# Kernel optimization log

Hardware: AMD Instinct MI355X
Metric: run time of the kernel (lower is better)

Reference implementation:

```python
import jax, jax.numpy as jnp
import numpy as np


def setup_inputs() -> dict:
    key = jax.random.key(0)
    k1, k2, k3, k4 = jax.random.split(key, 4)
    B, S, D, R = 8, 1024, 1024, 256
    batch = jax.random.normal(k1, (B, S, D), dtype=jnp.float32)
    proj_L = jax.random.uniform(k2, (D, R), dtype=jnp.float32, minval=-0.05, maxval=0.05)
    proj_R = jax.random.uniform(k3, (R, D), dtype=jnp.float32, minval=-0.05, maxval=0.05)
    bias = jax.random.uniform(k4, (1,), dtype=jnp.float32, minval=-0.05, maxval=0.05)
    return {"batch": batch, "proj_L": proj_L, "proj_R": proj_R, "bias": bias}


def reference(batch, proj_L, proj_R, bias):
    # logits[b,i,j] = h_i^T (L @ R) h_j + bias
    # Efficient factored form (same math, avoids O(B*S^2*D) intermediates):
    # left[b,i,r] = (batch @ L)[b,i,r]; right[b,j,r] = (batch @ R^T)[b,j,r]
    left = jnp.einsum('bid,dr->bir', batch, proj_L)    # (B,S,R)
    right = jnp.einsum('bjd,rd->bjr', batch, proj_R)   # (B,S,R)
    logits = jnp.einsum('bir,bjr->bij', left, right) + bias[0]
    return logits
```

## Files before the change

kernel.cpp:

```cpp
#include <hip/hip_runtime.h>

typedef __bf16 bf16_t;
typedef __bf16 bf16x8 __attribute__((ext_vector_type(8)));
typedef __bf16 bf16x4 __attribute__((ext_vector_type(4)));
typedef float f32x4 __attribute__((ext_vector_type(4)));

__device__ __forceinline__ void async16(const void* g, void* l) {
  __builtin_amdgcn_global_load_lds(
      (const __attribute__((address_space(1))) unsigned int*)g,
      (__attribute__((address_space(3))) unsigned int*)l,
      16, 0, 0);
}

__device__ __forceinline__ bf16x8 cvt8(const float4 a, const float4 b) {
  bf16x8 v;
  v[0] = (bf16_t)a.x; v[1] = (bf16_t)a.y; v[2] = (bf16_t)a.z; v[3] = (bf16_t)a.w;
  v[4] = (bf16_t)b.x; v[5] = (bf16_t)b.y; v[6] = (bf16_t)b.z; v[7] = (bf16_t)b.w;
  return v;
}

__global__ void prep_Bcat(const float* __restrict__ projL,
                          const float* __restrict__ projR,
                          bf16_t* __restrict__ Bcat) {
  const int t = threadIdx.x;
  if (blockIdx.x < 256) {
    int i = blockIdx.x * 256 + t;
    float4 v = ((const float4*)projR)[i];
    bf16x4 o;
    o[0] = (bf16_t)v.x; o[1] = (bf16_t)v.y; o[2] = (bf16_t)v.z; o[3] = (bf16_t)v.w;
    ((bf16x4*)(Bcat + (long)256 * 1024))[i] = o;
  } else {
    __shared__ float tile[32][33];
    const int bb = blockIdx.x - 256;
    const int n0 = (bb & 7) * 32;
    const int k0 = (bb >> 3) * 32;
    const int tx = t & 31;
    const int ty = t >> 5;
#pragma unroll
    for (int i = 0; i < 32; i += 8)
      tile[ty + i][tx] = projL[(long)(k0 + ty + i) * 256 + n0 + tx];
    __syncthreads();
#pragma unroll
    for (int i = 0; i < 32; i += 8)
      Bcat[(long)(n0 + ty + i) * 1024 + k0 + tx] = (bf16_t)tile[tx][ty + i];
  }
}

__global__ __launch_bounds__(256, 2) void gemm1_fusedA(
    const float* __restrict__ batch, const bf16_t* __restrict__ Bcat,
    bf16_t* __restrict__ LR) {
  const int bx = blockIdx.x;
  const int tm = (bx & 127) * 64;
  const int tn = (bx >> 7) * 128;

  __shared__ __attribute__((aligned(16))) bf16_t Bs[2 * 16384];

  const int t = threadIdx.x;
  const int lane = t & 63;
  const int quad = lane >> 4;
  const int l15 = lane & 15;
  const int wave = t >> 6;
  const int wr = (wave >> 1) * 32;
  const int wc = (wave & 1) * 64;

  const int rS = t >> 2;
  const int cS = (t & 3) * 8;
  const bf16_t* gB = Bcat + (long)(tn + rS) * 1024 + cS;

  const float* gA = batch + (long)(tm + wr + l15) * 1024 + quad * 8;

  f32x4 acc[2][4];
#pragma unroll
  for (int i = 0; i < 2; ++i)
#pragma unroll
    for (int j = 0; j < 4; ++j)
      acc[i][j] = (f32x4){0.f, 0.f, 0.f, 0.f};

#pragma unroll
  for (int kc = 0; kc < 4; ++kc) {
    async16(gB + kc * 32, Bs + kc * 4096 + t * 8);
    async16(gB + kc * 32 + (long)64 * 1024, Bs + kc * 4096 + 2048 + t * 8);
  }
  __syncthreads();

  for (int s = 0; s < 8; ++s) {
    const int buf = s & 1;
    const int nb = buf ^ 1;
    const int k0 = s * 128;
    if (s < 7) {
#pragma unroll
      for (int kc = 0; kc < 4; ++kc) {
        async16(gB + k0 + 128 + kc * 32, Bs + nb * 16384 + kc * 4096 + t * 8);
        async16(gB + k0 + 128 + kc * 32 + (long)64 * 1024,
                Bs + nb * 16384 + kc * 4096 + 2048 + t * 8);
      }
    }
    float4 a0[4][2], a1[4][2];
#pragma unroll
    for (int kc = 0; kc < 4; ++kc) {
      const float* p0 = gA + k0 + kc * 32;
      a0[kc][0] = *(const float4*)p0;
      a0[kc][1] = *(const float4*)(p0 + 4);
      const float* p1 = p0 + (long)16 * 1024;
      a1[kc][0] = *(const float4*)p1;
      a1[kc][1] = *(const float4*)(p1 + 4);
    }
#pragma unroll
    for (int kc = 0; kc < 4; ++kc) {
      bf16x8 af[2], bv[4];
      af[0] = cvt8(a0[kc][0], a0[kc][1]);
      af[1] = cvt8(a1[kc][0], a1[kc][1]);
      const bf16_t* Bk = Bs + buf * 16384 + kc * 4096;
#pragma unroll
      for (int j = 0; j < 4; ++j)
        bv[j] = *(const bf16x8*)(Bk + (wc + j * 16 + l15) * 32 + quad * 8);
#pragma unroll
      for (int i = 0; i < 2; ++i)
#pragma unroll
        for (int j = 0; j < 4; ++j)
          acc[i][j] = __builtin_amdgcn_mfma_f32_16x16x32_bf16(af[i], bv[j],
                                                              acc[i][j], 0, 0, 0);
    }
    __syncthreads();
  }

#pragma unroll
  for (int i = 0; i < 2; ++i) {
    const int r0 = tm + wr + i * 16 + quad * 4;
#pragma unroll
    for (int j = 0; j < 4; ++j) {
      const int c0 = tn + wc + j * 16 + l15;
#pragma unroll
      for (int r = 0; r < 4; ++r)
        LR[(long)(r0 + r) * 512 + c0] = (bf16_t)acc[i][j][r];
    }
  }
}

__global__ __launch_bounds__(256, 2) void gemm2(const bf16_t* __restrict__ LR,
                                                float* __restrict__ out,
                                                const float* __restrict__ bias) {
  const int bx = blockIdx.x;
  const int bz = bx & 7;
  const int tile = bx >> 3;
  const int tm = (tile & 7) * 128;
  const int tn = (tile >> 3) * 128;
  const bf16_t* LRb = LR + (long)bz * 1024 * 512;

  __shared__ __attribute__((aligned(16))) bf16_t As[2 * 8192];
  __shared__ __attribute__((aligned(16))) bf16_t Bs[2 * 8192];

  const int t = threadIdx.x;
  const int lane = t & 63;
  const int quad = lane >> 4;
  const int l15 = lane & 15;
  const int wave = t >> 6;
  const int wr = (wave >> 1) * 64;
  const int wc = (wave & 1) * 64;

  const int rS = t >> 2;
  const int cS = (t & 3) * 8;
  const bf16_t* gA = LRb + (long)(tm + rS) * 512 + cS;
  const bf16_t* gB = LRb + (long)(tn + rS) * 512 + 256 + cS;

  f32x4 acc[4][4];
#pragma unroll
  for (int i = 0; i < 4; ++i)
#pragma unroll
    for (int j = 0; j < 4; ++j)
      acc[i][j] = (f32x4){0.f, 0.f, 0.f, 0.f};

  auto STAGE = [&](int buf, int s) {
    const int k0 = s * 64;
    bf16_t* dA = As + buf * 8192 + t * 8;
    bf16_t* dB = Bs + buf * 8192 + t * 8;
#pragma unroll
    for (int kc = 0; kc < 2; ++kc) {
      const int ko = k0 + kc * 32;
      async16(gA + ko, dA + kc * 4096);
      async16(gA + ko + (long)64 * 512, dA + kc * 4096 + 2048);
      async16(gB + ko, dB + kc * 4096);
      async16(gB + ko + (long)64 * 512, dB + kc * 4096 + 2048);
    }
  };

  STAGE(0, 0);
  __syncthreads();

#pragma unroll
  for (int s = 0; s < 4; ++s) {
    if (s < 3) STAGE((s + 1) & 1, s + 1);
    const bf16_t* Ab = As + (s & 1) * 8192;
    const bf16_t* Bb = Bs + (s & 1) * 8192;
#pragma unroll
    for (int kc = 0; kc < 2; ++kc) {
      const bf16_t* Ak = Ab + kc * 4096;
      const bf16_t* Bk = Bb + kc * 4096;
      bf16x8 af[4], bv[4];
#pragma unroll
      for (int i = 0; i < 4; ++i)
        af[i] = *(const bf16x8*)(Ak + (wr + i * 16 + l15) * 32 + quad * 8);
#pragma unroll
      for (int j = 0; j < 4; ++j)
        bv[j] = *(const bf16x8*)(Bk + (wc + j * 16 + l15) * 32 + quad * 8);
#pragma unroll
      for (int i = 0; i < 4; ++i)
#pragma unroll
        for (int j = 0; j < 4; ++j)
          acc[i][j] = __builtin_amdgcn_mfma_f32_16x16x32_bf16(af[i], bv[j],
                                                              acc[i][j], 0, 0, 0);
    }
    if (s < 3) __syncthreads();
  }

  float* C = out + (long)bz * 1024 * 1024;
  const float bvadd = bias[0];
#pragma unroll
  for (int i = 0; i < 4; ++i) {
    const int r0 = tm + wr + i * 16 + quad * 4;
#pragma unroll
    for (int j = 0; j < 4; ++j) {
      const int c0 = tn + wc + j * 16 + l15;
#pragma unroll
      for (int r = 0; r < 4; ++r)
        C[(long)(r0 + r) * 1024 + c0] = acc[i][j][r] + bvadd;
    }
  }
}

extern "C" void kernel_launch(void* const* d_in, const int* in_sizes, int n_in,
                              void* d_out, int out_size, void* d_ws,
                              size_t ws_size, hipStream_t stream) {
  const float* batch = (const float*)d_in[0];
  const float* projL = (const float*)d_in[1];
  const float* projR = (const float*)d_in[2];
  const float* bias = (const float*)d_in[3];
  float* out = (float*)d_out;

  char* ws = (char*)d_ws;
  bf16_t* Bcat = (bf16_t*)ws;
  bf16_t* LR = (bf16_t*)(ws + (long)512 * 1024 * 2);

  prep_Bcat<<<512, 256, 0, stream>>>(projL, projR, Bcat);

  gemm1_fusedA<<<512, 256, 0, stream>>>(batch, Bcat, LR);

  gemm2<<<512, 256, 0, stream>>>(LR, out, bias);
}
```

Measured before the change: 132.4 us.

## Register double-buffer activation loads and relax stage barriers in gemm1

In gemm1, the fp32 activation tile for the next k-stage is now loaded into a second register buffer while the current stage's MFMAs run, instead of being loaded and used in the same stage. The full __syncthreads at each stage boundary becomes a partial `s_waitcnt vmcnt(8)` plus a raw barrier. This lets the next stage's register loads stay in flight across the barrier while the LDS B tile is guaranteed ready. The aim is to hide global-load latency on the main memory stream. The cost is roughly double the registers held for A prefetch, and the hand-counted vmcnt must match the issue order exactly.

After: 130.6 us. About the same (-1.3%).

```diff
diff --git a/kernel.cpp b/kernel.cpp
--- a/kernel.cpp
+++ b/kernel.cpp
@@ -76,41 +76,56 @@
     for (int j = 0; j < 4; ++j)
       acc[i][j] = (f32x4){0.f, 0.f, 0.f, 0.f};
 
+  float4 a0[2][4][2], a1[2][4][2];
+
 #pragma unroll
   for (int kc = 0; kc < 4; ++kc) {
     async16(gB + kc * 32, Bs + kc * 4096 + t * 8);
     async16(gB + kc * 32 + (long)64 * 1024, Bs + kc * 4096 + 2048 + t * 8);
   }
-  __syncthreads();
-
+  __builtin_amdgcn_sched_barrier(0);
+#pragma unroll
+  for (int kc = 0; kc < 4; ++kc) {
+    const float* p0 = gA + kc * 32;
+    a0[0][kc][0] = *(const float4*)p0;
+    a0[0][kc][1] = *(const float4*)(p0 + 4);
+    const float* p1 = p0 + (long)16 * 1024;
+    a1[0][kc][0] = *(const float4*)p1;
+    a1[0][kc][1] = *(const float4*)(p1 + 4);
+  }
+  asm volatile("s_waitcnt vmcnt(8)" ::: "memory");
+  __builtin_amdgcn_s_barrier();
+  __builtin_amdgcn_sched_barrier(0);
+
+#pragma unroll
   for (int s = 0; s < 8; ++s) {
-    const int buf = s & 1;
-    const int nb = buf ^ 1;
+    const int cur = s & 1;
+    const int nxt = cur ^ 1;
     const int k0 = s * 128;
     if (s < 7) {
 #pragma unroll
       for (int kc = 0; kc < 4; ++kc) {
-        async16(gB + k0 + 128 + kc * 32, Bs + nb * 16384 + kc * 4096 + t * 8);
+        async16(gB + k0 + 128 + kc * 32, Bs + nxt * 16384 + kc * 4096 + t * 8);
         async16(gB + k0 + 128 + kc * 32 + (long)64 * 1024,
-                Bs + nb * 16384 + kc * 4096 + 2048 + t * 8);
+                Bs + nxt * 16384 + kc * 4096 + 2048 + t * 8);
       }
-    }
-    float4 a0[4][2], a1[4][2];
-#pragma unroll
-    for (int kc = 0; kc < 4; ++kc) {
-      const float* p0 = gA + k0 + kc * 32;
-      a0[kc][0] = *(const float4*)p0;
-      a0[kc][1] = *(const float4*)(p0 + 4);
-      const float* p1 = p0 + (long)16 * 1024;
-      a1[kc][0] = *(const float4*)p1;
-      a1[kc][1] = *(const float4*)(p1 + 4);
+      __builtin_amdgcn_sched_barrier(0);
+#pragma unroll
+      for (int kc = 0; kc < 4; ++kc) {
+        const float* p0 = gA + k0 + 128 + kc * 32;
+        a0[nxt][kc][0] = *(const float4*)p0;
+        a0[nxt][kc][1] = *(const float4*)(p0 + 4);
+        const float* p1 = p0 + (long)16 * 1024;
+        a1[nxt][kc][0] = *(const float4*)p1;
+        a1[nxt][kc][1] = *(const float4*)(p1 + 4);
+      }
     }
 #pragma unroll
     for (int kc = 0; kc < 4; ++kc) {
       bf16x8 af[2], bv[4];
-      af[0] = cvt8(a0[kc][0], a0[kc][1]);
-      af[1] = cvt8(a1[kc][0], a1[kc][1]);
-      const bf16_t* Bk = Bs + buf * 16384 + kc * 4096;
+      af[0] = cvt8(a0[cur][kc][0], a0[cur][kc][1]);
+      af[1] = cvt8(a1[cur][kc][0], a1[cur][kc][1]);
+      const bf16_t* Bk = Bs + cur * 16384 + kc * 4096;
 #pragma unroll
       for (int j = 0; j < 4; ++j)
         bv[j] = *(const bf16x8*)(Bk + (wc + j * 16 + l15) * 32 + quad * 8);
@@ -121,7 +136,11 @@
           acc[i][j] = __builtin_amdgcn_mfma_f32_16x16x32_bf16(af[i], bv[j],
                                                               acc[i][j], 0, 0, 0);
     }
-    __syncthreads();
+    if (s < 7) {
+      asm volatile("s_waitcnt vmcnt(8)" ::: "memory");
+      __builtin_amdgcn_s_barrier();
+      __builtin_amdgcn_sched_barrier(0);
+    }
   }
 
 #pragma unroll
```

## Restage gemm1 A tile through LDS with smaller tiles and more blocks

Applied to the files above, without the earlier changes.

gemm1 drops its 64x128 tile for a 32x128 tile and launches 1024 blocks instead of 512, with launch bounds raised to 4 blocks per SM. The fp32 A tile is now read once with coalesced 64-byte-per-thread loads, converted to bf16 and staged in LDS, where all waves share it. Before, each wave read its own A rows from global memory with strided loads. The B tile loses its double buffer, so the B async loads now sit on the critical path before each barrier, and prefetch covers only the next A slab in registers. B tile traffic per output row doubles with the smaller M tile.

Result: faster. 115.1 us (-13.1%).

```diff
diff --git a/kernel.cpp b/kernel.cpp
--- a/kernel.cpp
+++ b/kernel.cpp
@@ -46,78 +46,79 @@
   }
 }
 
-__global__ __launch_bounds__(256, 2) void gemm1_fusedA(
+__global__ __launch_bounds__(256, 4) void gemm1_fusedA(
     const float* __restrict__ batch, const bf16_t* __restrict__ Bcat,
     bf16_t* __restrict__ LR) {
   const int bx = blockIdx.x;
-  const int tm = (bx & 127) * 64;
-  const int tn = (bx >> 7) * 128;
-
-  __shared__ __attribute__((aligned(16))) bf16_t Bs[2 * 16384];
+  const int tm = (bx & 255) * 32;
+  const int tn = (bx >> 8) * 128;
+
+  __shared__ __attribute__((aligned(16))) bf16_t As[4096];
+  __shared__ __attribute__((aligned(16))) bf16_t Bs[16384];
 
   const int t = threadIdx.x;
   const int lane = t & 63;
   const int quad = lane >> 4;
   const int l15 = lane & 15;
-  const int wave = t >> 6;
-  const int wr = (wave >> 1) * 32;
-  const int wc = (wave & 1) * 64;
+  const int w = t >> 6;
 
   const int rS = t >> 2;
   const int cS = (t & 3) * 8;
   const bf16_t* gB = Bcat + (long)(tn + rS) * 1024 + cS;
 
-  const float* gA = batch + (long)(tm + wr + l15) * 1024 + quad * 8;
-
-  f32x4 acc[2][4];
+  const int rA = t >> 3;
+  const int cA = (t & 7) * 16;
+  const float* gA = batch + (long)(tm + rA) * 1024 + cA;
+  bf16_t* lA = As + (cA >> 5) * 1024 + rA * 32 + (cA & 31);
+
+  f32x4 acc[2][2];
 #pragma unroll
   for (int i = 0; i < 2; ++i)
 #pragma unroll
-    for (int j = 0; j < 4; ++j)
+    for (int j = 0; j < 2; ++j)
       acc[i][j] = (f32x4){0.f, 0.f, 0.f, 0.f};
 
-#pragma unroll
-  for (int kc = 0; kc < 4; ++kc) {
-    async16(gB + kc * 32, Bs + kc * 4096 + t * 8);
-    async16(gB + kc * 32 + (long)64 * 1024, Bs + kc * 4096 + 2048 + t * 8);
-  }
-  __syncthreads();
+  float4 f0, f1, f2, f3;
+  f0 = *(const float4*)(gA + 0);
+  f1 = *(const float4*)(gA + 4);
+  f2 = *(const float4*)(gA + 8);
+  f3 = *(const float4*)(gA + 12);
 
   for (int s = 0; s < 8; ++s) {
-    const int buf = s & 1;
-    const int nb = buf ^ 1;
     const int k0 = s * 128;
+#pragma unroll
+    for (int kc = 0; kc < 4; ++kc) {
+      async16(gB + k0 + kc * 32, Bs + kc * 4096 + t * 8);
+      async16(gB + k0 + kc * 32 + (long)64 * 1024,
+              Bs + kc * 4096 + 2048 + t * 8);
+    }
+    *(bf16x8*)(lA) = cvt8(f0, f1);
+    *(bf16x8*)(lA + 8) = cvt8(f2, f3);
+    __syncthreads();
+
     if (s < 7) {
-#pragma unroll
-      for (int kc = 0; kc < 4; ++kc) {
-        async16(gB + k0 + 128 + kc * 32, Bs + nb * 16384 + kc * 4096 + t * 8);
-        async16(gB + k0 + 128 + kc * 32 + (long)64 * 1024,
-                Bs + nb * 16384 + kc * 4096 + 2048 + t * 8);
-      }
-    }
-    float4 a0[4][2], a1[4][2];
+      const float* p = gA + k0 + 128;
+      f0 = *(const float4*)(p + 0);
+      f1 = *(const float4*)(p + 4);
+      f2 = *(const float4*)(p + 8);
+      f3 = *(const float4*)(p + 12);
+    }
+
 #pragma unroll
     for (int kc = 0; kc < 4; ++kc) {
-      const float* p0 = gA + k0 + kc * 32;
-      a0[kc][0] = *(const float4*)p0;
-      a0[kc][1] = *(const float4*)(p0 + 4);
-      const float* p1 = p0 + (long)16 * 1024;
-      a1[kc][0] = *(const float4*)p1;
-      a1[kc][1] = *(const float4*)(p1 + 4);
-    }
-#pragma unroll
-    for (int kc = 0; kc < 4; ++kc) {
-      bf16x8 af[2], bv[4];
-      af[0] = cvt8(a0[kc][0], a0[kc][1]);
-      af[1] = cvt8(a1[kc][0], a1[kc][1]);
-      const bf16_t* Bk = Bs + buf * 16384 + kc * 4096;
-#pragma unroll
-      for (int j = 0; j < 4; ++j)
-        bv[j] = *(const bf16x8*)(Bk + (wc + j * 16 + l15) * 32 + quad * 8);
+      const bf16_t* Ak = As + kc * 1024;
+      const bf16_t* Bk = Bs + kc * 4096;
+      bf16x8 af[2], bv[2];
 #pragma unroll
       for (int i = 0; i < 2; ++i)
-#pragma unroll
-        for (int j = 0; j < 4; ++j)
+        af[i] = *(const bf16x8*)(Ak + (i * 16 + l15) * 32 + quad * 8);
+#pragma unroll
+      for (int j = 0; j < 2; ++j)
+        bv[j] = *(const bf16x8*)(Bk + (w * 32 + j * 16 + l15) * 32 + quad * 8);
+#pragma unroll
+      for (int i = 0; i < 2; ++i)
+#pragma unroll
+        for (int j = 0; j < 2; ++j)
           acc[i][j] = __builtin_amdgcn_mfma_f32_16x16x32_bf16(af[i], bv[j],
                                                               acc[i][j], 0, 0, 0);
     }
@@ -126,10 +127,10 @@
 
 #pragma unroll
   for (int i = 0; i < 2; ++i) {
-    const int r0 = tm + wr + i * 16 + quad * 4;
-#pragma unroll
-    for (int j = 0; j < 4; ++j) {
-      const int c0 = tn + wc + j * 16 + l15;
+    const int r0 = tm + i * 16 + quad * 4;
+#pragma unroll
+    for (int j = 0; j < 2; ++j) {
+      const int c0 = tn + w * 32 + j * 16 + l15;
 #pragma unroll
       for (int r = 0; r < 4; ++r)
         LR[(long)(r0 + r) * 512 + c0] = (bf16_t)acc[i][j][r];
@@ -243,7 +244,7 @@
 
   prep_Bcat<<<512, 256, 0, stream>>>(projL, projR, Bcat);
 
-  gemm1_fusedA<<<512, 256, 0, stream>>>(batch, Bcat, LR);
+  gemm1_fusedA<<<1024, 256, 0, stream>>>(batch, Bcat, LR);
 
   gemm2<<<512, 256, 0, stream>>>(LR, out, bias);
 }
```
